# Kernel tuning notes

Measured on AMD Instinct MI355X. Metric: run time of the kernel, lower is better.

The kernel has to match this reference:

```python
import jax, jax.numpy as jnp
import numpy as np

HEADS = 2
BN_EPS = 1e-5


def _axial_self_attn(x, Wq, Wkv, Wout, bout):
    # x: (b, s, t, c) -- attend along t (the axial sequence dim)
    b, s, t, c = x.shape
    dh = c // HEADS
    q = (x @ Wq).reshape(b, s, t, HEADS, dh)
    k, v = jnp.split(x @ Wkv, 2, axis=-1)  # matches torch .chunk(2, dim=-1)
    k = k.reshape(b, s, t, HEADS, dh)
    v = v.reshape(b, s, t, HEADS, dh)
    dots = jnp.einsum('bsind,bsjnd->bsnij', q, k) * (dh ** -0.5)
    attn = jax.nn.softmax(dots, axis=-1)
    out = jnp.einsum('bsnij,bsjnd->bsind', attn, v).reshape(b, s, t, c)
    return out @ Wout + bout


def setup_inputs() -> dict:
    key = jax.random.key(0)
    ks = jax.random.split(key, 8)
    B, C, H, W = 8, 128, 256, 256
    E = 2 * C
    sd = 0.05
    return {
        'x': jax.random.normal(ks[0], (B, C, H, W), jnp.float32),
        'Wq_h': jax.random.normal(ks[1], (C, C), jnp.float32) * sd,
        'Wkv_h': jax.random.normal(ks[2], (C, 2 * C), jnp.float32) * sd,
        'Wout_h': jax.random.normal(ks[3], (C, C), jnp.float32) * sd,
        'bout_h': jnp.zeros((C,), jnp.float32),
        'Wq_w': jax.random.normal(ks[4], (C, C), jnp.float32) * sd,
        'Wkv_w': jax.random.normal(ks[5], (C, 2 * C), jnp.float32) * sd,
        'Wout_w': jax.random.normal(ks[6], (C, C), jnp.float32) * sd,
        'bout_w': jnp.zeros((C,), jnp.float32),
        'conv_w': jax.random.normal(ks[7], (E, E), jnp.float32) * sd,  # (in, out); torch conv weight[o,i,0,0].T
        'gamma': jnp.ones((E,), jnp.float32),
        'beta': jnp.zeros((E,), jnp.float32),
    }


def reference(x, Wq_h, Wkv_h, Wout_h, bout_h, Wq_w, Wkv_w, Wout_w, bout_w, conv_w, gamma, beta):
    B, C, H, W = x.shape
    # MaxPool2d(2)
    xp = x.reshape(B, C, H // 2, 2, W // 2, 2).max(axis=(3, 5))  # (B,C,H2,W2)
    xc = jnp.transpose(xp, (0, 2, 3, 1))  # (B,H2,W2,C) channels-last
    # AxialAttention, sum_axial_out=True: height-axis attn + width-axis attn
    a_h = _axial_self_attn(jnp.transpose(xc, (0, 2, 1, 3)), Wq_h, Wkv_h, Wout_h, bout_h)
    a_h = jnp.transpose(a_h, (0, 2, 1, 3))
    a_w = _axial_self_attn(xc, Wq_w, Wkv_w, Wout_w, bout_w)
    a = jax.nn.relu(a_h + a_w)
    # cat((x_attn, x), dim=channel) then conv1x1 -> relu -> BatchNorm (batch stats)
    y = jnp.concatenate([a, xc], axis=-1) @ conv_w  # (B,H2,W2,2C)
    y = jax.nn.relu(y)
    mean = y.mean(axis=(0, 1, 2))
    var = y.var(axis=(0, 1, 2))
    y = (y - mean) * jax.lax.rsqrt(var + BN_EPS) * gamma + beta
    return jnp.transpose(y, (0, 3, 1, 2))  # back to NCHW
```

## Files before the change

kernel.cpp:

```cpp
#include <hip/hip_runtime.h>


typedef short v8s __attribute__((ext_vector_type(8)));
typedef short v4s __attribute__((ext_vector_type(4)));
typedef float v4f __attribute__((ext_vector_type(4)));
typedef float v4flt __attribute__((ext_vector_type(4)));

#define LSA 136
#define LSC 264
#define LSP 130

static __device__ __forceinline__ short f2bf(float f){
  unsigned u = __builtin_bit_cast(unsigned, f);
  u = (u + 0x7FFFu + ((u >> 16) & 1u)) >> 16;
  return (short)u;
}
static __device__ __forceinline__ float bf2f(short s){
  unsigned u = ((unsigned)(unsigned short)s) << 16;
  return __builtin_bit_cast(float, u);
}

__global__ void prep_kernel(const float* __restrict__ Wq_h, const float* __restrict__ Wkv_h,
                            const float* __restrict__ Wout_h, const float* __restrict__ Wq_w,
                            const float* __restrict__ Wkv_w, const float* __restrict__ Wout_w,
                            const float* __restrict__ conv_w, short* __restrict__ wt,
                            float* __restrict__ stats){
  int idx = blockIdx.x * 256 + threadIdx.x;
  if (idx < 8192) stats[idx] = 0.0f;
  const float* src; int K, O, base;
  if      (idx <  16384){ base = 0;      K=128; O=128; src=Wq_h;  }
  else if (idx <  49152){ base = 16384;  K=128; O=256; src=Wkv_h; }
  else if (idx <  65536){ base = 49152;  K=128; O=128; src=Wout_h;}
  else if (idx <  81920){ base = 65536;  K=128; O=128; src=Wq_w;  }
  else if (idx < 114688){ base = 81920;  K=128; O=256; src=Wkv_w; }
  else if (idx < 131072){ base = 114688; K=128; O=128; src=Wout_w;}
  else                  { base = 131072; K=256; O=256; src=conv_w;}
  int local = idx - base;
  int o = local / K, i = local - o * K;
  wt[idx] = f2bf(src[i * O + o]);
}

__global__ __launch_bounds__(256, 4)
void pool_kernel(const float* __restrict__ x, short* __restrict__ xp){
  __shared__ short t_[128*LSP];
  int bx = blockIdx.x;
  int b = bx >> 7, i = bx & 127;
  int tid = (int)threadIdx.x;
  int j2 = tid & 63;
  int cq = tid >> 6;
  for (int rep = 0; rep < 32; ++rep){
    int c = cq*32 + rep;
    const float* p0 = x + (((b*128 + c)*256 + 2*i)*256 + 4*j2);
    v4flt a  = *(const v4flt*)p0;
    v4flt bb = *(const v4flt*)(p0 + 256);
    t_[(2*j2)*LSP + c]   = f2bf(fmaxf(fmaxf(a[0], a[1]), fmaxf(bb[0], bb[1])));
    t_[(2*j2+1)*LSP + c] = f2bf(fmaxf(fmaxf(a[2], a[3]), fmaxf(bb[2], bb[3])));
  }
  __syncthreads();
  int obase = ((b*128 + i)*128)*128;
  for (int rep = 0; rep < 8; ++rep){
    int idx = rep*256 + tid;
    int row = idx >> 4, seg = idx & 15;
    *(v8s*)(xp + obase + row*128 + seg*8) = *(const v8s*)(&t_[row*LSP + seg*8]);
  }
}

__global__ __launch_bounds__(512, 2)
void attn_kernel(const short* __restrict__ xp, const short* __restrict__ wt,
                 const float* __restrict__ bout_h, const float* __restrict__ bout_w,
                 short* __restrict__ ah, short* __restrict__ aw){
  __shared__ short A[128*LSA];
  __shared__ short WB[128*LSA];

  const int bx = blockIdx.x;
  const int dir = bx & 1;
  const int sb = bx >> 1;
  const int b = sb >> 7, s = sb & 127;
  const int tid = (int)threadIdx.x;
  const int w = tid >> 6;
  const int lane = tid & 63;
  const int l15 = lane & 15, l4 = lane >> 4;

  const short* Wq   = wt + dir*65536;
  const short* Wk   = Wq + 16384;
  const short* Wv   = Wq + 32768;
  const short* Wout = Wq + 49152;
  const float* bsrc = dir ? bout_w : bout_h;
  short*       ao   = dir ? aw : ah;

  const int trow = 16*w + l15;
  const int xbase = dir ? (((b*128 + s)*128 + trow)*128)
                        : (((b*128 + trow)*128 + s)*128);
  v8s av[4];
  #pragma unroll
  for (int kk = 0; kk < 4; ++kk)
    av[kk] = *(const v8s*)(xp + xbase + kk*32 + l4*8);
  v8s wq_r[4], wk_r[4], wv_r[4], wo_r[4];
  #pragma unroll
  for (int r = 0; r < 4; ++r){
    int idx = (r*512 + tid) * 8;
    wq_r[r] = *(const v8s*)(Wq   + idx);
    wk_r[r] = *(const v8s*)(Wk   + idx);
    wv_r[r] = *(const v8s*)(Wv   + idx);
    wo_r[r] = *(const v8s*)(Wout + idx);
  }

#define STAGE_R(RG)                                                      \
  { _Pragma("unroll")                                                    \
    for (int r_ = 0; r_ < 4; ++r_){                                      \
      int idx_ = (r_*512 + tid) * 8;                                     \
      int oc_ = idx_ >> 7, ic_ = idx_ & 127;                             \
      *(v8s*)(&WB[oc_*LSA + ic_]) = RG[r_];                              \
    } }

  STAGE_R(wq_r);
  __syncthreads();

  #pragma unroll
  for (int tc = 0; tc < 8; ++tc){
    v4f d = {0.f,0.f,0.f,0.f};
    #pragma unroll
    for (int kk = 0; kk < 4; ++kk){
      v8s bf = *(const v8s*)(&WB[(tc*16 + l15)*LSA + kk*32 + l4*8]);
      d = __builtin_amdgcn_mfma_f32_16x16x32_bf16(av[kk], bf, d, 0, 0, 0);
    }
    #pragma unroll
    for (int r = 0; r < 4; ++r)
      A[(16*w + 4*l4 + r)*LSA + 16*tc + l15] = f2bf(d[r]);
  }
  v8s bq[2][2];
  #pragma unroll
  for (int h = 0; h < 2; ++h)
    #pragma unroll
    for (int kk = 0; kk < 2; ++kk)
      bq[h][kk] = *(const v8s*)(&A[(16*w + l15)*LSA + h*64 + kk*32 + l4*8]);
  __syncthreads();

  STAGE_R(wk_r);
  __syncthreads();

  #pragma unroll
  for (int tc = 0; tc < 8; ++tc){
    v4f d = {0.f,0.f,0.f,0.f};
    #pragma unroll
    for (int kk = 0; kk < 4; ++kk){
      v8s bf = *(const v8s*)(&WB[(tc*16 + l15)*LSA + kk*32 + l4*8]);
      d = __builtin_amdgcn_mfma_f32_16x16x32_bf16(av[kk], bf, d, 0, 0, 0);
    }
    #pragma unroll
    for (int r = 0; r < 4; ++r)
      A[(16*w + 4*l4 + r)*LSA + 16*tc + l15] = f2bf(d[r]);
  }
  __syncthreads();

  STAGE_R(wv_r);

  v4s pk[2][8];
  #pragma unroll
  for (int h = 0; h < 2; ++h){
    v4f st[8];
    #pragma unroll
    for (int jt = 0; jt < 8; ++jt){
      v4f d = {0.f,0.f,0.f,0.f};
      #pragma unroll
      for (int kk = 0; kk < 2; ++kk){
        v8s ak = *(const v8s*)(&A[(16*jt + l15)*LSA + h*64 + kk*32 + l4*8]);
        d = __builtin_amdgcn_mfma_f32_16x16x32_bf16(ak, bq[h][kk], d, 0, 0, 0);
      }
      st[jt] = d;
    }
    float mx = -1e30f;
    #pragma unroll
    for (int jt = 0; jt < 8; ++jt)
      #pragma unroll
      for (int r = 0; r < 4; ++r) mx = fmaxf(mx, st[jt][r]);
    mx = fmaxf(mx, __shfl_xor(mx, 16));
    mx = fmaxf(mx, __shfl_xor(mx, 32));
    float sm = 0.f;
    #pragma unroll
    for (int jt = 0; jt < 8; ++jt)
      #pragma unroll
      for (int r = 0; r < 4; ++r){
        float e = __expf((st[jt][r] - mx) * 0.125f);
        st[jt][r] = e; sm += e;
      }
    sm += __shfl_xor(sm, 16);
    sm += __shfl_xor(sm, 32);
    float inv = 1.0f / sm;
    #pragma unroll
    for (int jt = 0; jt < 8; ++jt)
      #pragma unroll
      for (int r = 0; r < 4; ++r) pk[h][jt][r] = f2bf(st[jt][r] * inv);
  }
  __syncthreads();

  v8s pa[2][4];
  #pragma unroll
  for (int h = 0; h < 2; ++h){
    #pragma unroll
    for (int jt = 0; jt < 8; ++jt)
      *(v4s*)(&A[(16*w + l15)*LSA + 16*jt + 4*l4]) = pk[h][jt];
    #pragma unroll
    for (int kk = 0; kk < 4; ++kk)
      pa[h][kk] = *(const v8s*)(&A[(16*w + l15)*LSA + kk*32 + l4*8]);
  }
  __syncthreads();

  #pragma unroll
  for (int tc = 0; tc < 8; ++tc){
    v4f d = {0.f,0.f,0.f,0.f};
    #pragma unroll
    for (int kk = 0; kk < 4; ++kk){
      v8s bf = *(const v8s*)(&WB[(tc*16 + l15)*LSA + kk*32 + l4*8]);
      d = __builtin_amdgcn_mfma_f32_16x16x32_bf16(av[kk], bf, d, 0, 0, 0);
    }
    v4s pkv;
    #pragma unroll
    for (int r = 0; r < 4; ++r) pkv[r] = f2bf(d[r]);
    *(v4s*)(&A[(16*tc + l15)*LSA + 16*w + 4*l4]) = pkv;
  }
  __syncthreads();

  STAGE_R(wo_r);

  v4f ot[2][4];
  #pragma unroll
  for (int h = 0; h < 2; ++h)
    #pragma unroll
    for (int tc = 0; tc < 4; ++tc){
      v4f d = {0.f,0.f,0.f,0.f};
      #pragma unroll
      for (int kk = 0; kk < 4; ++kk){
        v8s vf = *(const v8s*)(&A[(64*h + 16*tc + l15)*LSA + kk*32 + l4*8]);
        d = __builtin_amdgcn_mfma_f32_16x16x32_bf16(vf, pa[h][kk], d, 0, 0, 0);
      }
      ot[h][tc] = d;
    }
  __syncthreads();

  #pragma unroll
  for (int h = 0; h < 2; ++h)
    #pragma unroll
    for (int tc = 0; tc < 4; ++tc){
      v4s pko;
      #pragma unroll
      for (int r = 0; r < 4; ++r) pko[r] = f2bf(ot[h][tc][r]);
      *(v4s*)(&A[(16*w + l15)*LSA + 64*h + 16*tc + 4*l4]) = pko;
    }
  v8s ob[4];
  #pragma unroll
  for (int kk = 0; kk < 4; ++kk)
    ob[kk] = *(const v8s*)(&A[(16*w + l15)*LSA + kk*32 + l4*8]);
  #pragma unroll
  for (int tc = 0; tc < 8; ++tc){
    v4f d = {0.f,0.f,0.f,0.f};
    #pragma unroll
    for (int kk = 0; kk < 4; ++kk){
      v8s awf = *(const v8s*)(&WB[(tc*16 + l15)*LSA + kk*32 + l4*8]);
      d = __builtin_amdgcn_mfma_f32_16x16x32_bf16(awf, ob[kk], d, 0, 0, 0);
    }
    v4f bias = *(const v4f*)(bsrc + 16*tc + 4*l4);
    v4s z;
    #pragma unroll
    for (int r = 0; r < 4; ++r) z[r] = f2bf(d[r] + bias[r]);
    *(v4s*)(&A[(16*w + l15)*LSA + 16*tc + 4*l4]) = z;
  }
  __syncthreads();

  int obase = ((b*128 + s)*128)*128;
  #pragma unroll
  for (int r = 0; r < 4; ++r){
    int idx = (r*512 + tid) * 8;
    int t = idx >> 7, c = idx & 127;
    *(v8s*)(ao + obase + t*128 + c) = *(const v8s*)(&A[t*LSA + c]);
  }
#undef STAGE_R
}

__global__ __launch_bounds__(512, 2)
void conv_kernel(const short* __restrict__ ah, const short* __restrict__ aw,
                 const short* __restrict__ xp, const short* __restrict__ wt,
                 short* __restrict__ yb, float* __restrict__ stats){
  __shared__ short cats[128*LSC];
  __shared__ float lsum[256];
  __shared__ float lsq[256];
  const short* convT = wt + 131072;
  int bx = blockIdx.x;
  int b = bx >> 7, ii = bx & 127;
  int tid = (int)threadIdx.x;
  int wv = tid >> 6, lane = tid & 63, l15 = lane & 15, l4 = lane >> 4;
  if (tid < 256){ lsum[tid] = 0.f; lsq[tid] = 0.f; }

  v8s wf[2][8];
  #pragma unroll
  for (int x = 0; x < 2; ++x)
    #pragma unroll
    for (int kk = 0; kk < 8; ++kk)
      wf[x][kk] = *(const v8s*)(convT + (((wv + 8*x)*16 + l15)*256) + kk*32 + l4*8);

  for (int r = 0; r < 4; ++r){
    int idx = (r*512 + tid) * 8;
    int t = idx >> 7, c = idx & 127;
    v8s hv = *(const v8s*)(ah + ((b*128 + t)*128 + ii)*128 + c);
    v8s wv_ = *(const v8s*)(aw + ((b*128 + ii)*128 + t)*128 + c);
    v8s o;
    #pragma unroll
    for (int k = 0; k < 8; ++k)
      o[k] = f2bf(fmaxf(bf2f(hv[k]) + bf2f(wv_[k]), 0.f));
    *(v8s*)(&cats[t*LSC + c]) = o;
    *(v8s*)(&cats[t*LSC + 128 + c]) =
        *(const v8s*)(xp + ((b*128 + ii)*128 + t)*128 + c);
  }
  __syncthreads();

  v4s ypk[2][8];
  float s1[2] = {0.f,0.f}, s2[2] = {0.f,0.f};
  #pragma unroll
  for (int tt = 0; tt < 8; ++tt){
    v4f d0 = {0.f,0.f,0.f,0.f}, d1 = {0.f,0.f,0.f,0.f};
    #pragma unroll
    for (int kk = 0; kk < 8; ++kk){
      v8s af = *(const v8s*)(&cats[(16*tt + l15)*LSC + kk*32 + l4*8]);
      d0 = __builtin_amdgcn_mfma_f32_16x16x32_bf16(af, wf[0][kk], d0, 0, 0, 0);
      d1 = __builtin_amdgcn_mfma_f32_16x16x32_bf16(af, wf[1][kk], d1, 0, 0, 0);
    }
    #pragma unroll
    for (int r = 0; r < 4; ++r){
      float y0 = fmaxf(d0[r], 0.f), y1 = fmaxf(d1[r], 0.f);
      ypk[0][tt][r] = f2bf(y0); ypk[1][tt][r] = f2bf(y1);
      s1[0] += y0; s2[0] += y0*y0;
      s1[1] += y1; s2[1] += y1*y1;
    }
  }
  #pragma unroll
  for (int x = 0; x < 2; ++x){
    s1[x] += __shfl_xor(s1[x], 16); s1[x] += __shfl_xor(s1[x], 32);
    s2[x] += __shfl_xor(s2[x], 16); s2[x] += __shfl_xor(s2[x], 32);
  }
  if (l4 == 0){
    #pragma unroll
    for (int x = 0; x < 2; ++x){
      int e = (wv + 8*x)*16 + l15;
      atomicAdd(&lsum[e], s1[x]);
      atomicAdd(&lsq[e],  s2[x]);
    }
  }
  __syncthreads();
  #pragma unroll
  for (int x = 0; x < 2; ++x)
    #pragma unroll
    for (int tt = 0; tt < 8; ++tt)
      *(v4s*)(&cats[((wv + 8*x)*16 + l15)*132 + 16*tt + 4*l4]) = ypk[x][tt];
  __syncthreads();
  for (int r = 0; r < 8; ++r){
    int idx = (r*512 + tid) * 8;
    int e = idx >> 7, j = idx & 127;
    *(v8s*)(yb + ((b*256 + e)*128 + ii)*128 + j) = *(const v8s*)(&cats[e*132 + j]);
  }
  if (tid < 256){
    int c = bx & 15;
    atomicAdd(&stats[c*512 + tid],       lsum[tid]);
    atomicAdd(&stats[c*512 + 256 + tid], lsq[tid]);
  }
}

__global__ void bn_kernel(const short* __restrict__ yb, float* __restrict__ out,
                          const float* __restrict__ stats,
                          const float* __restrict__ gamma, const float* __restrict__ beta){
  const float invn = 1.0f / 131072.0f;
  int bx = blockIdx.x;
  int e = bx & 255;
  float s1 = 0.f, s2 = 0.f;
  #pragma unroll
  for (int c = 0; c < 16; ++c){
    s1 += stats[c*512 + e];
    s2 += stats[c*512 + 256 + e];
  }
  float m   = s1 * invn;
  float var = s2 * invn - m * m;
  float sc  = gamma[e] * rsqrtf(var + 1e-5f);
  float sh  = beta[e] - m * sc;
  int base = bx * 16384;
  int tid = (int)threadIdx.x;
  for (int rep = 0; rep < 8; ++rep){
    int idx = base + (rep*256 + tid)*8;
    v8s yv = *(const v8s*)(yb + idx);
    v4f o1, o2;
    #pragma unroll
    for (int r = 0; r < 4; ++r){
      o1[r] = bf2f(yv[r])   * sc + sh;
      o2[r] = bf2f(yv[4+r]) * sc + sh;
    }
    *(v4f*)(out + idx)     = o1;
    *(v4f*)(out + idx + 4) = o2;
  }
}

extern "C" void kernel_launch(void* const* d_in, const int* in_sizes, int n_in,
                              void* d_out, int out_size, void* d_ws, size_t ws_size,
                              hipStream_t stream){
  const float* x      = (const float*)d_in[0];
  const float* Wq_h   = (const float*)d_in[1];
  const float* Wkv_h  = (const float*)d_in[2];
  const float* Wout_h = (const float*)d_in[3];
  const float* bout_h = (const float*)d_in[4];
  const float* Wq_w   = (const float*)d_in[5];
  const float* Wkv_w  = (const float*)d_in[6];
  const float* Wout_w = (const float*)d_in[7];
  const float* bout_w = (const float*)d_in[8];
  const float* conv_w = (const float*)d_in[9];
  const float* gamma  = (const float*)d_in[10];
  const float* beta   = (const float*)d_in[11];
  float* out = (float*)d_out;

  char* ws = (char*)d_ws;
  short* xp    = (short*)(ws);
  short* ah    = (short*)(ws +  33554432);
  short* aw    = (short*)(ws +  67108864);
  short* yb    = (short*)(ws + 100663296);
  short* wt    = (short*)(ws + 167772160);
  float* stats = (float*)(ws + 168165376);

  prep_kernel<<<768, 256, 0, stream>>>(Wq_h, Wkv_h, Wout_h, Wq_w, Wkv_w, Wout_w,
                                       conv_w, wt, stats);
  pool_kernel<<<1024, 256, 0, stream>>>(x, xp);
  attn_kernel<<<2048, 512, 0, stream>>>(xp, wt, bout_h, bout_w, ah, aw);
  conv_kernel<<<1024, 512, 0, stream>>>(ah, aw, xp, wt, yb, stats);
  bn_kernel<<<2048, 256, 0, stream>>>(yb, out, stats, gamma, beta);
}
```

Measured before the change: 287.4 us.

## Stage attention weights in half-tiles to cut LDS and registers for higher occupancy

The attention kernel no longer preloads all four weight matrices into registers up front. Each weight is now loaded from global memory in two 64-row halves into a half-sized shared buffer, with the projection GEMMs split to match. The launch bound is raised from 2 to 6 blocks per CU. The aim is to lower LDS use and register pressure so more blocks can be resident. The cost is several extra barriers and global loads that now sit on the critical path, no longer prefetched.

```diff
diff --git a/kernel.cpp b/kernel.cpp
--- a/kernel.cpp
+++ b/kernel.cpp
@@ -65,12 +65,12 @@
   }
 }
 
-__global__ __launch_bounds__(512, 2)
+__global__ __launch_bounds__(512, 6)
 void attn_kernel(const short* __restrict__ xp, const short* __restrict__ wt,
                  const float* __restrict__ bout_h, const float* __restrict__ bout_w,
                  short* __restrict__ ah, short* __restrict__ aw){
   __shared__ short A[128*LSA];
-  __shared__ short WB[128*LSA];
+  __shared__ short WB[64*LSA];
 
   const int bx = blockIdx.x;
   const int dir = bx & 1;
@@ -95,39 +95,35 @@
   #pragma unroll
   for (int kk = 0; kk < 4; ++kk)
     av[kk] = *(const v8s*)(xp + xbase + kk*32 + l4*8);
-  v8s wq_r[4], wk_r[4], wv_r[4], wo_r[4];
-  #pragma unroll
-  for (int r = 0; r < 4; ++r){
-    int idx = (r*512 + tid) * 8;
-    wq_r[r] = *(const v8s*)(Wq   + idx);
-    wk_r[r] = *(const v8s*)(Wk   + idx);
-    wv_r[r] = *(const v8s*)(Wv   + idx);
-    wo_r[r] = *(const v8s*)(Wout + idx);
-  }
-
-#define STAGE_R(RG)                                                      \
+
+#define STAGE_H(SRC, HF)                                                 \
   { _Pragma("unroll")                                                    \
-    for (int r_ = 0; r_ < 4; ++r_){                                      \
-      int idx_ = (r_*512 + tid) * 8;                                     \
-      int oc_ = idx_ >> 7, ic_ = idx_ & 127;                             \
-      *(v8s*)(&WB[oc_*LSA + ic_]) = RG[r_];                              \
+    for (int r_ = 0; r_ < 2; ++r_){                                      \
+      int idx_ = r_*512 + tid;                              \
+      int oc_ = idx_ >> 4, seg_ = idx_ & 15;                             \
+      *(v8s*)(&WB[oc_*LSA + seg_*8]) =                                   \
+          *(const v8s*)((SRC) + (64*(HF) + oc_)*128 + seg_*8);           \
     } }
 
-  STAGE_R(wq_r);
-  __syncthreads();
-
-  #pragma unroll
-  for (int tc = 0; tc < 8; ++tc){
-    v4f d = {0.f,0.f,0.f,0.f};
-    #pragma unroll
-    for (int kk = 0; kk < 4; ++kk){
-      v8s bf = *(const v8s*)(&WB[(tc*16 + l15)*LSA + kk*32 + l4*8]);
-      d = __builtin_amdgcn_mfma_f32_16x16x32_bf16(av[kk], bf, d, 0, 0, 0);
-    }
-    #pragma unroll
-    for (int r = 0; r < 4; ++r)
-      A[(16*w + 4*l4 + r)*LSA + 16*tc + l15] = f2bf(d[r]);
-  }
+#define QK_HALF(HF)                                                      \
+  { _Pragma("unroll")                                                    \
+    for (int tcl = 0; tcl < 4; ++tcl){                                   \
+      int tc = 4*(HF) + tcl;                                             \
+      v4f d = {0.f,0.f,0.f,0.f};                                         \
+      _Pragma("unroll")                                                  \
+      for (int kk = 0; kk < 4; ++kk){                                    \
+        v8s bf = *(const v8s*)(&WB[(tcl*16 + l15)*LSA + kk*32 + l4*8]);  \
+        d = __builtin_amdgcn_mfma_f32_16x16x32_bf16(av[kk], bf, d, 0, 0, 0); \
+      }                                                                  \
+      _Pragma("unroll")                                                  \
+      for (int r = 0; r < 4; ++r)                                        \
+        A[(16*w + 4*l4 + r)*LSA + 16*tc + l15] = f2bf(d[r]);             \
+    } }
+
+  STAGE_H(Wq, 0); __syncthreads();
+  QK_HALF(0);     __syncthreads();
+  STAGE_H(Wq, 1); __syncthreads();
+  QK_HALF(1);
   v8s bq[2][2];
   #pragma unroll
   for (int h = 0; h < 2; ++h)
@@ -136,24 +132,12 @@
       bq[h][kk] = *(const v8s*)(&A[(16*w + l15)*LSA + h*64 + kk*32 + l4*8]);
   __syncthreads();
 
-  STAGE_R(wk_r);
-  __syncthreads();
-
-  #pragma unroll
-  for (int tc = 0; tc < 8; ++tc){
-    v4f d = {0.f,0.f,0.f,0.f};
-    #pragma unroll
-    for (int kk = 0; kk < 4; ++kk){
-      v8s bf = *(const v8s*)(&WB[(tc*16 + l15)*LSA + kk*32 + l4*8]);
-      d = __builtin_amdgcn_mfma_f32_16x16x32_bf16(av[kk], bf, d, 0, 0, 0);
-    }
-    #pragma unroll
-    for (int r = 0; r < 4; ++r)
-      A[(16*w + 4*l4 + r)*LSA + 16*tc + l15] = f2bf(d[r]);
-  }
-  __syncthreads();
-
-  STAGE_R(wv_r);
+  STAGE_H(Wk, 0); __syncthreads();
+  QK_HALF(0);     __syncthreads();
+  STAGE_H(Wk, 1); __syncthreads();
+  QK_HALF(1);     __syncthreads();
+
+  STAGE_H(Wv, 0);
 
   v4s pk[2][8];
   #pragma unroll
@@ -207,11 +191,12 @@
   __syncthreads();
 
   #pragma unroll
-  for (int tc = 0; tc < 8; ++tc){
+  for (int tcl = 0; tcl < 4; ++tcl){
+    int tc = tcl;
     v4f d = {0.f,0.f,0.f,0.f};
     #pragma unroll
     for (int kk = 0; kk < 4; ++kk){
-      v8s bf = *(const v8s*)(&WB[(tc*16 + l15)*LSA + kk*32 + l4*8]);
+      v8s bf = *(const v8s*)(&WB[(tcl*16 + l15)*LSA + kk*32 + l4*8]);
       d = __builtin_amdgcn_mfma_f32_16x16x32_bf16(av[kk], bf, d, 0, 0, 0);
     }
     v4s pkv;
@@ -220,8 +205,24 @@
     *(v4s*)(&A[(16*tc + l15)*LSA + 16*w + 4*l4]) = pkv;
   }
   __syncthreads();
-
-  STAGE_R(wo_r);
+  STAGE_H(Wv, 1); __syncthreads();
+  #pragma unroll
+  for (int tcl = 0; tcl < 4; ++tcl){
+    int tc = 4 + tcl;
+    v4f d = {0.f,0.f,0.f,0.f};
+    #pragma unroll
+    for (int kk = 0; kk < 4; ++kk){
+      v8s bf = *(const v8s*)(&WB[(tcl*16 + l15)*LSA + kk*32 + l4*8]);
+      d = __builtin_amdgcn_mfma_f32_16x16x32_bf16(av[kk], bf, d, 0, 0, 0);
+    }
+    v4s pkv;
+    #pragma unroll
+    for (int r = 0; r < 4; ++r) pkv[r] = f2bf(d[r]);
+    *(v4s*)(&A[(16*tc + l15)*LSA + 16*w + 4*l4]) = pkv;
+  }
+  __syncthreads();
+
+  STAGE_H(Wout, 0);
 
   v4f ot[2][4];
   #pragma unroll
@@ -251,20 +252,28 @@
   #pragma unroll
   for (int kk = 0; kk < 4; ++kk)
     ob[kk] = *(const v8s*)(&A[(16*w + l15)*LSA + kk*32 + l4*8]);
-  #pragma unroll
-  for (int tc = 0; tc < 8; ++tc){
-    v4f d = {0.f,0.f,0.f,0.f};
-    #pragma unroll
-    for (int kk = 0; kk < 4; ++kk){
-      v8s awf = *(const v8s*)(&WB[(tc*16 + l15)*LSA + kk*32 + l4*8]);
-      d = __builtin_amdgcn_mfma_f32_16x16x32_bf16(awf, ob[kk], d, 0, 0, 0);
-    }
-    v4f bias = *(const v4f*)(bsrc + 16*tc + 4*l4);
-    v4s z;
-    #pragma unroll
-    for (int r = 0; r < 4; ++r) z[r] = f2bf(d[r] + bias[r]);
-    *(v4s*)(&A[(16*w + l15)*LSA + 16*tc + 4*l4]) = z;
-  }
+
+#define OUTPROJ_HALF(HF)                                                 \
+  { _Pragma("unroll")                                                    \
+    for (int tcl = 0; tcl < 4; ++tcl){                                   \
+      int tc = 4*(HF) + tcl;                                             \
+      v4f d = {0.f,0.f,0.f,0.f};                                         \
+      _Pragma("unroll")                                                  \
+      for (int kk = 0; kk < 4; ++kk){                                    \
+        v8s awf = *(const v8s*)(&WB[(tcl*16 + l15)*LSA + kk*32 + l4*8]); \
+        d = __builtin_amdgcn_mfma_f32_16x16x32_bf16(awf, ob[kk], d, 0, 0, 0); \
+      }                                                                  \
+      v4f bias = *(const v4f*)(bsrc + 16*tc + 4*l4);                     \
+      v4s z;                                                             \
+      _Pragma("unroll")                                                  \
+      for (int r = 0; r < 4; ++r) z[r] = f2bf(d[r] + bias[r]);           \
+      *(v4s*)(&A[(16*w + l15)*LSA + 16*tc + 4*l4]) = z;                  \
+    } }
+
+  OUTPROJ_HALF(0);
+  __syncthreads();
+  STAGE_H(Wout, 1); __syncthreads();
+  OUTPROJ_HALF(1);
   __syncthreads();
 
   int obase = ((b*128 + s)*128)*128;
@@ -274,7 +283,9 @@
     int t = idx >> 7, c = idx & 127;
     *(v8s*)(ao + obase + t*128 + c) = *(const v8s*)(&A[t*LSA + c]);
   }
-#undef STAGE_R
+#undef STAGE_H
+#undef QK_HALF
+#undef OUTPROJ_HALF
 }
 
 __global__ __launch_bounds__(512, 2)
```

After: 274.3 us. 4.6% less time.
